# Kernel tuning notes

Hardware: AMD Instinct MI355X
Metric: run time of the kernel (lower is better)

The kernel has to match this reference:

```python
import jax, jax.numpy as jnp
import numpy as np

N, M, IN_DIM, OUT_DIM = 32768, 8192, 256, 64


def setup_inputs() -> dict:
    key = jax.random.key(0)
    k1, k2, k3, k4 = jax.random.split(key, 4)
    H = jax.random.bernoulli(k1, 0.01, (N, M)).astype(jnp.float32)
    w = jax.random.uniform(k2, (M,), minval=0.5, maxval=1.5, dtype=jnp.float32)
    x = jax.random.normal(k3, (N, IN_DIM), dtype=jnp.float32)
    W_lin = jax.random.normal(k4, (IN_DIM, OUT_DIM), dtype=jnp.float32) * (1.0 / np.sqrt(IN_DIM))
    b_lin = jnp.zeros((OUT_DIM,), dtype=jnp.float32)
    return {"x": x, "H": H, "w": w, "W_lin": W_lin, "b_lin": b_lin}


def reference(x, H, w, W_lin, b_lin):
    # Theta = Dv^{-1/2} H diag(w) De^{-1} H^T Dv^{-1/2}; out = Theta @ (x W + b).
    # Applied right-to-left with O(N) diagonal broadcasts instead of materializing
    # the [N, N] operator -- identical math to the torch reference.
    De = jnp.clip(jnp.sum(H, axis=0), 1.0, None)                 # [M] edge degrees
    Dv = jnp.clip(jnp.sum(H * w[None, :], axis=1), 1e-6, None)   # [N] weighted node degrees
    dv_inv_sqrt = Dv ** -0.5                                     # [N]
    y = x @ W_lin + b_lin                                        # [N, out]
    t = H.T @ (dv_inv_sqrt[:, None] * y)                         # [M, out] gather to edges
    t = (w / De)[:, None] * t                                    # edge scaling W De^{-1}
    out = dv_inv_sqrt[:, None] * (H @ t)                         # [N, out] scatter back
    return out
```

## Files before the change

kernel.cpp:

```cpp
#include <hip/hip_runtime.h>

#define N_NODES 32768
#define M_EDGES 8192
#define IN_DIM  256
#define OUT_F   64

#define SCAN_ROWS 16
#define NBLK   (N_NODES / SCAN_ROWS)
#define RBCAP  192
#define COLCAP 512

__global__ __launch_bounds__(256) void k_scan(const float* __restrict__ H,
                                              unsigned short* __restrict__ rowidx,
                                              unsigned* __restrict__ rowlen) {
    int tid  = threadIdx.x;
    int lane = tid & 63;
    int wid  = tid >> 6;
    int row0 = blockIdx.x * SCAN_ROWS;

    for (int rr = wid; rr < SCAN_ROWS; rr += 4) {
        int n = row0 + rr;
        const float4* Hrow = (const float4*)(H + (size_t)n * M_EDGES);
        unsigned short* out_r = rowidx + (size_t)n * RBCAP;

        unsigned mreg[4];
        #pragma unroll
        for (int ob = 0; ob < 4; ++ob) {
            int jb = ob * 512;
            float4 h0 = Hrow[jb + lane];
            float4 h1 = Hrow[jb + 64  + lane];
            float4 h2 = Hrow[jb + 128 + lane];
            float4 h3 = Hrow[jb + 192 + lane];
            float4 h4 = Hrow[jb + 256 + lane];
            float4 h5 = Hrow[jb + 320 + lane];
            float4 h6 = Hrow[jb + 384 + lane];
            float4 h7 = Hrow[jb + 448 + lane];
            unsigned mk = 0;
            #define PK(hv, g)                                                  \
            {                                                                  \
                unsigned b = (unsigned)(hv.x != 0.f)                           \
                           | ((unsigned)(hv.y != 0.f) << 1)                    \
                           | ((unsigned)(hv.z != 0.f) << 2)                    \
                           | ((unsigned)(hv.w != 0.f) << 3);                   \
                mk |= b << (4 * (g));                                          \
            }
            PK(h0, 0) PK(h1, 1) PK(h2, 2) PK(h3, 3)
            PK(h4, 4) PK(h5, 5) PK(h6, 6) PK(h7, 7)
            #undef PK
            mreg[ob] = mk;
        }

        unsigned cnt = (unsigned)(__popc(mreg[0]) + __popc(mreg[1])
                                + __popc(mreg[2]) + __popc(mreg[3]));
        unsigned incl = cnt;
        #pragma unroll
        for (int off = 1; off < 64; off <<= 1) {
            unsigned v = (unsigned)__shfl_up((int)incl, off, 64);
            if (lane >= off) incl += v;
        }
        unsigned pos = incl - cnt;
        unsigned total = (unsigned)__shfl((int)incl, 63, 64);

        #pragma unroll
        for (int r = 0; r < 4; ++r) {
            unsigned m = mreg[r];
            while (m) {
                int p = __ffs(m) - 1;
                int g = p >> 2;
                int c = p & 3;
                int m_idx = r * 2048 + g * 256 + (lane << 2) + c;
                if (pos < RBCAP) out_r[pos] = (unsigned short)m_idx;
                ++pos;
                m &= m - 1;
            }
        }
        if (lane == 63)
            rowlen[n] = (total < (unsigned)RBCAP) ? total : (unsigned)RBCAP;
    }
}

__global__ __launch_bounds__(256) void k_csc(const unsigned short* __restrict__ rowidx,
                                             const unsigned* __restrict__ rowlen,
                                             const float* __restrict__ w,
                                             unsigned short* __restrict__ cscidx,
                                             unsigned* __restrict__ cscfill,
                                             float* __restrict__ Dv_raw) {
    int lane = threadIdx.x & 63;
    int wid  = threadIdx.x >> 6;
    int n = blockIdx.x * 4 + wid;
    unsigned cnt = rowlen[n];
    float dv = 0.f;
    for (unsigned j = lane; j < cnt; j += 64) {
        int m = rowidx[(size_t)n * RBCAP + j];
        dv += w[m];
        unsigned p = atomicAdd(&cscfill[m], 1u);
        if (p < (unsigned)COLCAP)
            cscidx[(size_t)m * COLCAP + p] = (unsigned short)n;
    }
    for (int off = 32; off; off >>= 1) dv += __shfl_down(dv, off, 64);
    if (lane == 0) Dv_raw[n] = dv;
}

__global__ __launch_bounds__(256) void k_lin(const float* __restrict__ x,
                                             const float* __restrict__ Wl,
                                             const float* __restrict__ b,
                                             const float* __restrict__ Dv_raw,
                                             float* __restrict__ y2) {
    __shared__ float x_s[16 * IN_DIM];
    int tid = threadIdx.x;
    int n0 = blockIdx.x * 16;
    for (int i = tid; i < 16 * IN_DIM; i += 256)
        x_s[i] = x[(size_t)n0 * IN_DIM + i];
    __syncthreads();
    int k = tid & 63;
    int rbase = tid >> 6;
    for (int pass = 0; pass < 4; ++pass) {
        int r = pass * 4 + rbase;
        float acc = b[k];
        const float* xr = x_s + r * IN_DIM;
        #pragma unroll 8
        for (int i = 0; i < IN_DIM; ++i)
            acc = fmaf(xr[i], Wl[i * OUT_F + k], acc);
        float dvis = rsqrtf(fmaxf(Dv_raw[n0 + r], 1e-6f));
        y2[(size_t)(n0 + r) * OUT_F + k] = acc * dvis;
    }
}

#define SEG_GATHER(vi, base, cnt, src, acc0, acc1, acc2, acc3, acc4, acc5, acc6, acc7) \
{                                                                              \
    unsigned end = ((cnt) > (base)) ? ((cnt) - (base)) : 0u;                   \
    if (end > 64u) end = 64u;                                                  \
    unsigned sj = 0;                                                           \
    for (; sj + 8 <= end; sj += 8) {                                           \
        int m0 = __builtin_amdgcn_readlane(vi, sj + 0);                        \
        int m1 = __builtin_amdgcn_readlane(vi, sj + 1);                        \
        int m2 = __builtin_amdgcn_readlane(vi, sj + 2);                        \
        int m3 = __builtin_amdgcn_readlane(vi, sj + 3);                        \
        int m4 = __builtin_amdgcn_readlane(vi, sj + 4);                        \
        int m5 = __builtin_amdgcn_readlane(vi, sj + 5);                        \
        int m6 = __builtin_amdgcn_readlane(vi, sj + 6);                        \
        int m7 = __builtin_amdgcn_readlane(vi, sj + 7);                        \
        acc0 += src[(size_t)m0 * OUT_F + lane];                                \
        acc1 += src[(size_t)m1 * OUT_F + lane];                                \
        acc2 += src[(size_t)m2 * OUT_F + lane];                                \
        acc3 += src[(size_t)m3 * OUT_F + lane];                                \
        acc4 += src[(size_t)m4 * OUT_F + lane];                                \
        acc5 += src[(size_t)m5 * OUT_F + lane];                                \
        acc6 += src[(size_t)m6 * OUT_F + lane];                                \
        acc7 += src[(size_t)m7 * OUT_F + lane];                                \
    }                                                                          \
    for (; sj < end; ++sj) {                                                   \
        int mm = __builtin_amdgcn_readlane(vi, sj);                            \
        acc0 += src[(size_t)mm * OUT_F + lane];                                \
    }                                                                          \
}

__global__ __launch_bounds__(256) void k_edge(const unsigned short* __restrict__ cscidx,
                                              const unsigned* __restrict__ cscfill,
                                              const float* __restrict__ w,
                                              const float* __restrict__ y2,
                                              float* __restrict__ t) {
    int lane = threadIdx.x & 63;
    int wid  = threadIdx.x >> 6;
    int m = blockIdx.x * 4 + wid;
    unsigned de = cscfill[m];
    unsigned cnt = (de < (unsigned)COLCAP) ? de : (unsigned)COLCAP;
    const unsigned short* cp = cscidx + (size_t)m * COLCAP;
    int v0 = cp[lane];         int v1 = cp[64  + lane];
    int v2 = cp[128 + lane];   int v3 = cp[192 + lane];
    int v4 = cp[256 + lane];   int v5 = cp[320 + lane];
    int v6 = cp[384 + lane];   int v7 = cp[448 + lane];
    float a0 = 0.f, a1 = 0.f, a2 = 0.f, a3 = 0.f;
    float a4 = 0.f, a5 = 0.f, a6 = 0.f, a7 = 0.f;
    SEG_GATHER(v0,   0u, cnt, y2, a0, a1, a2, a3, a4, a5, a6, a7)
    SEG_GATHER(v1,  64u, cnt, y2, a0, a1, a2, a3, a4, a5, a6, a7)
    SEG_GATHER(v2, 128u, cnt, y2, a0, a1, a2, a3, a4, a5, a6, a7)
    SEG_GATHER(v3, 192u, cnt, y2, a0, a1, a2, a3, a4, a5, a6, a7)
    SEG_GATHER(v4, 256u, cnt, y2, a0, a1, a2, a3, a4, a5, a6, a7)
    SEG_GATHER(v5, 320u, cnt, y2, a0, a1, a2, a3, a4, a5, a6, a7)
    SEG_GATHER(v6, 384u, cnt, y2, a0, a1, a2, a3, a4, a5, a6, a7)
    SEG_GATHER(v7, 448u, cnt, y2, a0, a1, a2, a3, a4, a5, a6, a7)
    float acc = ((a0 + a1) + (a2 + a3)) + ((a4 + a5) + (a6 + a7));
    float sc = w[m] / fmaxf((float)de, 1.0f);
    t[(size_t)m * OUT_F + lane] = acc * sc;
}

__global__ __launch_bounds__(256) void k_out(const unsigned short* __restrict__ rowidx,
                                             const unsigned* __restrict__ rowlen,
                                             const float* __restrict__ t,
                                             const float* __restrict__ Dv_raw,
                                             float* __restrict__ out) {
    int lane = threadIdx.x & 63;
    int wid  = threadIdx.x >> 6;
    int n = blockIdx.x * 4 + wid;
    unsigned cnt = rowlen[n];
    const unsigned short* rp = rowidx + (size_t)n * RBCAP;
    int v0 = rp[lane];
    int v1 = rp[64  + lane];
    int v2 = rp[128 + lane];
    float a0 = 0.f, a1 = 0.f, a2 = 0.f, a3 = 0.f;
    float a4 = 0.f, a5 = 0.f, a6 = 0.f, a7 = 0.f;
    SEG_GATHER(v0,   0u, cnt, t, a0, a1, a2, a3, a4, a5, a6, a7)
    SEG_GATHER(v1,  64u, cnt, t, a0, a1, a2, a3, a4, a5, a6, a7)
    SEG_GATHER(v2, 128u, cnt, t, a0, a1, a2, a3, a4, a5, a6, a7)
    float acc = ((a0 + a1) + (a2 + a3)) + ((a4 + a5) + (a6 + a7));
    float dvis = rsqrtf(fmaxf(Dv_raw[n], 1e-6f));
    out[(size_t)n * OUT_F + lane] = dvis * acc;
}

extern "C" void kernel_launch(void* const* d_in, const int* in_sizes, int n_in,
                              void* d_out, int out_size, void* d_ws, size_t ws_size,
                              hipStream_t stream) {
    const float* x  = (const float*)d_in[0];
    const float* H  = (const float*)d_in[1];
    const float* w  = (const float*)d_in[2];
    const float* Wl = (const float*)d_in[3];
    const float* bl = (const float*)d_in[4];
    float* out = (float*)d_out;

    float*    y2      = (float*)d_ws;
    float*    t       = y2 + (size_t)N_NODES * OUT_F;
    float*    Dv_raw  = t + (size_t)M_EDGES * OUT_F;
    unsigned* rowlen  = (unsigned*)(Dv_raw + N_NODES);
    unsigned* cscfill = rowlen + N_NODES;
    unsigned short* rowidx = (unsigned short*)(cscfill + M_EDGES);
    unsigned short* cscidx = rowidx + (size_t)N_NODES * RBCAP;

    hipMemsetAsync(cscfill, 0, M_EDGES * sizeof(unsigned), stream);

    k_scan<<<dim3(NBLK),         dim3(256), 0, stream>>>(H, rowidx, rowlen);
    k_csc <<<dim3(N_NODES / 4),  dim3(256), 0, stream>>>(rowidx, rowlen, w, cscidx, cscfill, Dv_raw);
    k_lin <<<dim3(N_NODES / 16), dim3(256), 0, stream>>>(x, Wl, bl, Dv_raw, y2);
    k_edge<<<dim3(M_EDGES / 4),  dim3(256), 0, stream>>>(cscidx, cscfill, w, y2, t);
    k_out <<<dim3(N_NODES / 4),  dim3(256), 0, stream>>>(rowidx, rowlen, t, Dv_raw, out);
}
```

Before: 1.587 ms.

## Fuse CSC build into scan and gather float4 rows in edge/out kernels

Folds the CSC construction and weighted node-degree computation into the H scan kernel, removing one launch and the re-read of the row index lists. The edge and output gather kernels now have each wave handle four neighbours at once, with 16 lanes loading float4 slices of a row and a cross-lane shuffle reduction at the end, replacing the scalar readlane loop. In exchange, the scan kernel's inner loop now issues atomics and scattered writes, which could slow the bandwidth-bound scan of H. The gathers also add masking and shuffle overhead.

```diff
diff --git a/kernel.cpp b/kernel.cpp
--- a/kernel.cpp
+++ b/kernel.cpp
@@ -11,8 +11,12 @@
 #define COLCAP 512
 
 __global__ __launch_bounds__(256) void k_scan(const float* __restrict__ H,
+                                              const float* __restrict__ w,
                                               unsigned short* __restrict__ rowidx,
-                                              unsigned* __restrict__ rowlen) {
+                                              unsigned* __restrict__ rowlen,
+                                              unsigned short* __restrict__ cscidx,
+                                              unsigned* __restrict__ cscfill,
+                                              float* __restrict__ Dv_raw) {
     int tid  = threadIdx.x;
     int lane = tid & 63;
     int wid  = tid >> 6;
@@ -61,44 +65,29 @@
         unsigned pos = incl - cnt;
         unsigned total = (unsigned)__shfl((int)incl, 63, 64);
 
+        float dv = 0.f;
         #pragma unroll
         for (int r = 0; r < 4; ++r) {
-            unsigned m = mreg[r];
-            while (m) {
-                int p = __ffs(m) - 1;
+            unsigned mm = mreg[r];
+            while (mm) {
+                int p = __ffs(mm) - 1;
                 int g = p >> 2;
-                int c = p & 3;
-                int m_idx = r * 2048 + g * 256 + (lane << 2) + c;
+                int c4 = p & 3;
+                int m_idx = r * 2048 + g * 256 + (lane << 2) + c4;
                 if (pos < RBCAP) out_r[pos] = (unsigned short)m_idx;
                 ++pos;
-                m &= m - 1;
+                dv += w[m_idx];
+                unsigned fp = atomicAdd(&cscfill[m_idx], 1u);
+                if (fp < (unsigned)COLCAP)
+                    cscidx[(size_t)m_idx * COLCAP + fp] = (unsigned short)n;
+                mm &= mm - 1;
             }
         }
+        for (int off = 32; off; off >>= 1) dv += __shfl_down(dv, off, 64);
+        if (lane == 0) Dv_raw[n] = dv;
         if (lane == 63)
             rowlen[n] = (total < (unsigned)RBCAP) ? total : (unsigned)RBCAP;
     }
-}
-
-__global__ __launch_bounds__(256) void k_csc(const unsigned short* __restrict__ rowidx,
-                                             const unsigned* __restrict__ rowlen,
-                                             const float* __restrict__ w,
-                                             unsigned short* __restrict__ cscidx,
-                                             unsigned* __restrict__ cscfill,
-                                             float* __restrict__ Dv_raw) {
-    int lane = threadIdx.x & 63;
-    int wid  = threadIdx.x >> 6;
-    int n = blockIdx.x * 4 + wid;
-    unsigned cnt = rowlen[n];
-    float dv = 0.f;
-    for (unsigned j = lane; j < cnt; j += 64) {
-        int m = rowidx[(size_t)n * RBCAP + j];
-        dv += w[m];
-        unsigned p = atomicAdd(&cscfill[m], 1u);
-        if (p < (unsigned)COLCAP)
-            cscidx[(size_t)m * COLCAP + p] = (unsigned short)n;
-    }
-    for (int off = 32; off; off >>= 1) dv += __shfl_down(dv, off, 64);
-    if (lane == 0) Dv_raw[n] = dv;
 }
 
 __global__ __launch_bounds__(256) void k_lin(const float* __restrict__ x,
@@ -126,32 +115,20 @@
     }
 }
 
-#define SEG_GATHER(vi, base, cnt, src, acc0, acc1, acc2, acc3, acc4, acc5, acc6, acc7) \
-{                                                                              \
-    unsigned end = ((cnt) > (base)) ? ((cnt) - (base)) : 0u;                   \
-    if (end > 64u) end = 64u;                                                  \
-    unsigned sj = 0;                                                           \
-    for (; sj + 8 <= end; sj += 8) {                                           \
-        int m0 = __builtin_amdgcn_readlane(vi, sj + 0);                        \
-        int m1 = __builtin_amdgcn_readlane(vi, sj + 1);                        \
-        int m2 = __builtin_amdgcn_readlane(vi, sj + 2);                        \
-        int m3 = __builtin_amdgcn_readlane(vi, sj + 3);                        \
-        int m4 = __builtin_amdgcn_readlane(vi, sj + 4);                        \
-        int m5 = __builtin_amdgcn_readlane(vi, sj + 5);                        \
-        int m6 = __builtin_amdgcn_readlane(vi, sj + 6);                        \
-        int m7 = __builtin_amdgcn_readlane(vi, sj + 7);                        \
-        acc0 += src[(size_t)m0 * OUT_F + lane];                                \
-        acc1 += src[(size_t)m1 * OUT_F + lane];                                \
-        acc2 += src[(size_t)m2 * OUT_F + lane];                                \
-        acc3 += src[(size_t)m3 * OUT_F + lane];                                \
-        acc4 += src[(size_t)m4 * OUT_F + lane];                                \
-        acc5 += src[(size_t)m5 * OUT_F + lane];                                \
-        acc6 += src[(size_t)m6 * OUT_F + lane];                                \
-        acc7 += src[(size_t)m7 * OUT_F + lane];                                \
-    }                                                                          \
-    for (; sj < end; ++sj) {                                                   \
-        int mm = __builtin_amdgcn_readlane(vi, sj);                            \
-        acc0 += src[(size_t)mm * OUT_F + lane];                                \
+#define SEGQ(vi, base, cnt, src, ax, ay, az, aw, g, c, lane)                   \
+if ((base) < (cnt)) {                                                          \
+    unsigned rem = (cnt) - (base); if (rem > 64u) rem = 64u;                   \
+    unsigned nq = (rem + 3u) >> 2;                                             \
+    _Pragma("unroll 4")                                                        \
+    for (unsigned qq = 0; qq < nq; ++qq) {                                     \
+        int nidx = __shfl(vi, (int)(4u * qq) + (g), 64);                       \
+        const float4* srcp = (const float4*)((src) + (size_t)nidx * OUT_F);    \
+        float4 v = srcp[c];                                                    \
+        bool ok = (4u * qq + (unsigned)(g)) < rem;                             \
+        ax += ok ? v.x : 0.f;                                                  \
+        ay += ok ? v.y : 0.f;                                                  \
+        az += ok ? v.z : 0.f;                                                  \
+        aw += ok ? v.w : 0.f;                                                  \
     }                                                                          \
 }
 
@@ -166,23 +143,30 @@
     unsigned de = cscfill[m];
     unsigned cnt = (de < (unsigned)COLCAP) ? de : (unsigned)COLCAP;
     const unsigned short* cp = cscidx + (size_t)m * COLCAP;
+    int g = lane >> 4;
+    int c = lane & 15;
     int v0 = cp[lane];         int v1 = cp[64  + lane];
     int v2 = cp[128 + lane];   int v3 = cp[192 + lane];
     int v4 = cp[256 + lane];   int v5 = cp[320 + lane];
     int v6 = cp[384 + lane];   int v7 = cp[448 + lane];
-    float a0 = 0.f, a1 = 0.f, a2 = 0.f, a3 = 0.f;
-    float a4 = 0.f, a5 = 0.f, a6 = 0.f, a7 = 0.f;
-    SEG_GATHER(v0,   0u, cnt, y2, a0, a1, a2, a3, a4, a5, a6, a7)
-    SEG_GATHER(v1,  64u, cnt, y2, a0, a1, a2, a3, a4, a5, a6, a7)
-    SEG_GATHER(v2, 128u, cnt, y2, a0, a1, a2, a3, a4, a5, a6, a7)
-    SEG_GATHER(v3, 192u, cnt, y2, a0, a1, a2, a3, a4, a5, a6, a7)
-    SEG_GATHER(v4, 256u, cnt, y2, a0, a1, a2, a3, a4, a5, a6, a7)
-    SEG_GATHER(v5, 320u, cnt, y2, a0, a1, a2, a3, a4, a5, a6, a7)
-    SEG_GATHER(v6, 384u, cnt, y2, a0, a1, a2, a3, a4, a5, a6, a7)
-    SEG_GATHER(v7, 448u, cnt, y2, a0, a1, a2, a3, a4, a5, a6, a7)
-    float acc = ((a0 + a1) + (a2 + a3)) + ((a4 + a5) + (a6 + a7));
-    float sc = w[m] / fmaxf((float)de, 1.0f);
-    t[(size_t)m * OUT_F + lane] = acc * sc;
+    float ax = 0.f, ay = 0.f, az = 0.f, aw = 0.f;
+    SEGQ(v0,   0u, cnt, y2, ax, ay, az, aw, g, c, lane)
+    SEGQ(v1,  64u, cnt, y2, ax, ay, az, aw, g, c, lane)
+    SEGQ(v2, 128u, cnt, y2, ax, ay, az, aw, g, c, lane)
+    SEGQ(v3, 192u, cnt, y2, ax, ay, az, aw, g, c, lane)
+    SEGQ(v4, 256u, cnt, y2, ax, ay, az, aw, g, c, lane)
+    SEGQ(v5, 320u, cnt, y2, ax, ay, az, aw, g, c, lane)
+    SEGQ(v6, 384u, cnt, y2, ax, ay, az, aw, g, c, lane)
+    SEGQ(v7, 448u, cnt, y2, ax, ay, az, aw, g, c, lane)
+    ax += __shfl_xor(ax, 16, 64); ax += __shfl_xor(ax, 32, 64);
+    ay += __shfl_xor(ay, 16, 64); ay += __shfl_xor(ay, 32, 64);
+    az += __shfl_xor(az, 16, 64); az += __shfl_xor(az, 32, 64);
+    aw += __shfl_xor(aw, 16, 64); aw += __shfl_xor(aw, 32, 64);
+    if (g == 0) {
+        float sc = w[m] / fmaxf((float)de, 1.0f);
+        float4 r4 = { ax * sc, ay * sc, az * sc, aw * sc };
+        ((float4*)(t + (size_t)m * OUT_F))[c] = r4;
+    }
 }
 
 __global__ __launch_bounds__(256) void k_out(const unsigned short* __restrict__ rowidx,
@@ -195,17 +179,24 @@
     int n = blockIdx.x * 4 + wid;
     unsigned cnt = rowlen[n];
     const unsigned short* rp = rowidx + (size_t)n * RBCAP;
+    int g = lane >> 4;
+    int c = lane & 15;
     int v0 = rp[lane];
     int v1 = rp[64  + lane];
     int v2 = rp[128 + lane];
-    float a0 = 0.f, a1 = 0.f, a2 = 0.f, a3 = 0.f;
-    float a4 = 0.f, a5 = 0.f, a6 = 0.f, a7 = 0.f;
-    SEG_GATHER(v0,   0u, cnt, t, a0, a1, a2, a3, a4, a5, a6, a7)
-    SEG_GATHER(v1,  64u, cnt, t, a0, a1, a2, a3, a4, a5, a6, a7)
-    SEG_GATHER(v2, 128u, cnt, t, a0, a1, a2, a3, a4, a5, a6, a7)
-    float acc = ((a0 + a1) + (a2 + a3)) + ((a4 + a5) + (a6 + a7));
-    float dvis = rsqrtf(fmaxf(Dv_raw[n], 1e-6f));
-    out[(size_t)n * OUT_F + lane] = dvis * acc;
+    float ax = 0.f, ay = 0.f, az = 0.f, aw = 0.f;
+    SEGQ(v0,   0u, cnt, t, ax, ay, az, aw, g, c, lane)
+    SEGQ(v1,  64u, cnt, t, ax, ay, az, aw, g, c, lane)
+    SEGQ(v2, 128u, cnt, t, ax, ay, az, aw, g, c, lane)
+    ax += __shfl_xor(ax, 16, 64); ax += __shfl_xor(ax, 32, 64);
+    ay += __shfl_xor(ay, 16, 64); ay += __shfl_xor(ay, 32, 64);
+    az += __shfl_xor(az, 16, 64); az += __shfl_xor(az, 32, 64);
+    aw += __shfl_xor(aw, 16, 64); aw += __shfl_xor(aw, 32, 64);
+    if (g == 0) {
+        float dvis = rsqrtf(fmaxf(Dv_raw[n], 1e-6f));
+        float4 r4 = { ax * dvis, ay * dvis, az * dvis, aw * dvis };
+        ((float4*)(out + (size_t)n * OUT_F))[c] = r4;
+    }
 }
 
 extern "C" void kernel_launch(void* const* d_in, const int* in_sizes, int n_in,
@@ -228,8 +219,7 @@
 
     hipMemsetAsync(cscfill, 0, M_EDGES * sizeof(unsigned), stream);
 
-    k_scan<<<dim3(NBLK),         dim3(256), 0, stream>>>(H, rowidx, rowlen);
-    k_csc <<<dim3(N_NODES / 4),  dim3(256), 0, stream>>>(rowidx, rowlen, w, cscidx, cscfill, Dv_raw);
+    k_scan<<<dim3(NBLK),         dim3(256), 0, stream>>>(H, w, rowidx, rowlen, cscidx, cscfill, Dv_raw);
     k_lin <<<dim3(N_NODES / 16), dim3(256), 0, stream>>>(x, Wl, bl, Dv_raw, y2);
     k_edge<<<dim3(M_EDGES / 4),  dim3(256), 0, stream>>>(cscidx, cscfill, w, y2, t);
     k_out <<<dim3(N_NODES / 4),  dim3(256), 0, stream>>>(rowidx, rowlen, t, Dv_raw, out);
```

Result: faster. 1.538 ms (median of 2 runs) (-3.1%).
